# Optimization experiments

Measured on AMD Instinct MI355X. Metric: run time of the kernel, lower is better.

Reference implementation:

```python
import jax, jax.numpy as jnp
import numpy as np

THRESHOLD = 0.1   # init_kwargs threshold
CACHELINE = 64    # init_kwargs cacheline_size


def _cluster_line(line):
    """Serial near-duplicate clustering within one cacheline.

    Semantics of cluster_img's inner loops: walk the line left to right;
    each value is snapped to the FIRST earlier 'base' within THRESHOLD,
    otherwise it becomes a new base itself.
    """
    C = line.shape[0]
    slot = jnp.arange(C, dtype=jnp.int32)

    def step(carry, val):
        bases, n = carry  # bases: [C] values, n: number of valid bases
        mask = (jnp.abs(bases - val) < THRESHOLD) & (slot < n)
        has = mask.any()
        idx = jnp.argmax(mask)             # first matching base
        out = jnp.where(has, bases[idx], val)
        appended = jnp.where(slot == n, val, bases)
        bases = jnp.where(has, bases, appended)
        n = n + jnp.where(has, jnp.int32(0), jnp.int32(1))
        return (bases, n), out

    (_, _), outs = jax.lax.scan(
        step, (jnp.zeros(C, line.dtype), jnp.int32(0)), line)
    return outs


def _cluster(x):
    shape = x.shape
    flat = x.reshape(-1)
    n_lines = flat.shape[0] // CACHELINE
    head = flat[: n_lines * CACHELINE].reshape(n_lines, CACHELINE)
    clustered = jax.vmap(_cluster_line)(head).reshape(-1)
    # elements past the last full cacheline are left unchanged (while-loop tail)
    out = jnp.concatenate([clustered, flat[n_lines * CACHELINE:]])
    return out.reshape(shape)


def setup_inputs() -> dict:
    key = jax.random.key(0)
    x = jax.random.normal(key, (64, 64, 112, 112), dtype=jnp.float32)
    return {"x": x}


def reference(x):
    return _cluster(x)
```

## Files before the change

kernel.cpp:

```cpp
#include <hip/hip_runtime.h>

#define THRESH 0.1f
#define LINE 64

__global__ __launch_bounds__(256, 8) void cluster_kernel(
    const float* __restrict__ in, float* __restrict__ out,
    long long n_lines, long long total)
{
    const int lane = threadIdx.x & 63;
    const long long n_waves = ((long long)gridDim.x * blockDim.x) >> 6;
    long long line = ((long long)blockIdx.x * blockDim.x + threadIdx.x) >> 6;

    if (line < n_lines) {
        float x = in[line * LINE + lane];
        for (;;) {
            const long long next = line + n_waves;
            float xn = 0.0f;
            if (next < n_lines) xn = in[next * LINE + lane];

            float o = x;
            bool covered = false;
            unsigned long long uncovered = ~0ULL;
            while (uncovered) {
                int b = __ffsll(uncovered) - 1;
                b = __builtin_amdgcn_readfirstlane(b);
                const float base =
                    __int_as_float(__builtin_amdgcn_readlane(__float_as_int(x), b));
                const bool m = (!covered) && (fabsf(x - base) < THRESH);
                if (m) { o = base; covered = true; }
                uncovered &= ~__ballot(m);
            }
            out[line * LINE + lane] = o;

            if (next >= n_lines) break;
            x = xn;
            line = next;
        }
    }

    const long long tail_start = n_lines * LINE;
    for (long long i = tail_start + (long long)blockIdx.x * blockDim.x + threadIdx.x;
         i < total; i += (long long)gridDim.x * blockDim.x) {
        out[i] = in[i];
    }
}

extern "C" void kernel_launch(void* const* d_in, const int* in_sizes, int n_in,
                              void* d_out, int out_size, void* d_ws, size_t ws_size,
                              hipStream_t stream) {
    const float* x = (const float*)d_in[0];
    float* out = (float*)d_out;
    const long long total = (long long)in_sizes[0];
    const long long n_lines = total / LINE;

    const int block = 256;
    const int grid = 2048;
    cluster_kernel<<<grid, block, 0, stream>>>(x, out, n_lines, total);
}
```

Baseline: 553.6 us.

## Interleave two cachelines per wave in hand-written asm clustering loop

Each wavefront now processes two cachelines at once. Their serial base-selection loops run interleaved in inline GCN assembly (readlane, compare, cndmask, ff1) to expose instruction-level parallelism across the two independent dependency chains. The hand-scheduled asm also removes compiler-generated overhead from the per-iteration loop. The trade-off is that each pair runs for the longer of the two lines' iteration counts, and explicit s_nop hazard padding is added.

Result: faster. 471.0 us (-14.9%).

```diff
diff --git a/kernel.cpp b/kernel.cpp
--- a/kernel.cpp
+++ b/kernel.cpp
@@ -1,59 +1,101 @@
 #include <hip/hip_runtime.h>
 
-#define THRESH 0.1f
 #define LINE 64
+
+__device__ __forceinline__ void cluster_pair(float xA, float xB, float thr,
+                                             float& oA_out, float& oB_out) {
+  float oA = xA, oB = xB;
+  float dA, dB, vbA, vbB;
+  float sbA, sbB;
+  unsigned long long unA, unB;
+  int bA, bB;
+  asm volatile(
+      "s_mov_b64 %[unA], -1\n\t"
+      "s_mov_b64 %[unB], -1\n\t"
+      "s_mov_b32 %[bA], 0\n\t"
+      "s_mov_b32 %[bB], 0\n\t"
+      "1:\n\t"
+      "v_readlane_b32 %[sbA], %[xA], %[bA]\n\t"
+      "v_readlane_b32 %[sbB], %[xB], %[bB]\n\t"
+      "s_nop 1\n\t"
+      "v_mov_b32 %[vbA], %[sbA]\n\t"
+      "v_mov_b32 %[vbB], %[sbB]\n\t"
+      "v_sub_f32 %[dA], %[vbA], %[xA]\n\t"
+      "v_cmp_gt_f32 vcc, %[t], abs(%[dA])\n\t"
+      "s_and_b64 vcc, vcc, %[unA]\n\t"
+      "v_cndmask_b32 %[oA], %[oA], %[vbA], vcc\n\t"
+      "s_andn2_b64 %[unA], %[unA], vcc\n\t"
+      "s_ff1_i32_b64 %[bA], %[unA]\n\t"
+      "v_sub_f32 %[dB], %[vbB], %[xB]\n\t"
+      "v_cmp_gt_f32 vcc, %[t], abs(%[dB])\n\t"
+      "s_and_b64 vcc, vcc, %[unB]\n\t"
+      "v_cndmask_b32 %[oB], %[oB], %[vbB], vcc\n\t"
+      "s_andn2_b64 %[unB], %[unB], vcc\n\t"
+      "s_ff1_i32_b64 %[bB], %[unB]\n\t"
+      "s_or_b64 vcc, %[unA], %[unB]\n\t"
+      "s_cbranch_scc1 1b\n\t"
+      : [oA] "+v"(oA), [oB] "+v"(oB),
+        [dA] "=&v"(dA), [dB] "=&v"(dB),
+        [vbA] "=&v"(vbA), [vbB] "=&v"(vbB),
+        [sbA] "=&s"(sbA), [sbB] "=&s"(sbB),
+        [unA] "=&s"(unA), [unB] "=&s"(unB),
+        [bA] "=&s"(bA), [bB] "=&s"(bB)
+      : [xA] "v"(xA), [xB] "v"(xB), [t] "s"(thr)
+      : "vcc", "scc");
+  oA_out = oA;
+  oB_out = oB;
+}
 
 __global__ __launch_bounds__(256, 8) void cluster_kernel(
     const float* __restrict__ in, float* __restrict__ out,
     long long n_lines, long long total)
 {
-    const int lane = threadIdx.x & 63;
-    const long long n_waves = ((long long)gridDim.x * blockDim.x) >> 6;
-    long long line = ((long long)blockIdx.x * blockDim.x + threadIdx.x) >> 6;
+  const int lane = threadIdx.x & 63;
+  const long long wid = ((long long)blockIdx.x * blockDim.x + threadIdx.x) >> 6;
+  const long long n_waves = ((long long)gridDim.x * blockDim.x) >> 6;
+  const long long n_pairs = (n_lines + 1) >> 1;
 
-    if (line < n_lines) {
-        float x = in[line * LINE + lane];
-        for (;;) {
-            const long long next = line + n_waves;
-            float xn = 0.0f;
-            if (next < n_lines) xn = in[next * LINE + lane];
+  long long pair = wid;
+  if (pair < n_pairs) {
+    long long lA = 2 * pair, lB = 2 * pair + 1;
+    float xA = in[lA * LINE + lane];
+    float xB = (lB < n_lines) ? in[lB * LINE + lane] : xA;
+    for (;;) {
+      const long long np = pair + n_waves;
+      const bool has_next = np < n_pairs;
+      float xA2 = 0.f, xB2 = 0.f;
+      if (has_next) {
+        const long long nA = 2 * np, nB = 2 * np + 1;
+        xA2 = in[nA * LINE + lane];
+        xB2 = (nB < n_lines) ? in[nB * LINE + lane] : xA2;
+      }
 
-            float o = x;
-            bool covered = false;
-            unsigned long long uncovered = ~0ULL;
-            while (uncovered) {
-                int b = __ffsll(uncovered) - 1;
-                b = __builtin_amdgcn_readfirstlane(b);
-                const float base =
-                    __int_as_float(__builtin_amdgcn_readlane(__float_as_int(x), b));
-                const bool m = (!covered) && (fabsf(x - base) < THRESH);
-                if (m) { o = base; covered = true; }
-                uncovered &= ~__ballot(m);
-            }
-            out[line * LINE + lane] = o;
+      float oA, oB;
+      cluster_pair(xA, xB, 0.1f, oA, oB);
 
-            if (next >= n_lines) break;
-            x = xn;
-            line = next;
-        }
+      out[2 * pair * LINE + lane] = oA;
+      if (2 * pair + 1 < n_lines) out[(2 * pair + 1) * LINE + lane] = oB;
+
+      if (!has_next) break;
+      xA = xA2; xB = xB2; pair = np;
     }
+  }
 
-    const long long tail_start = n_lines * LINE;
-    for (long long i = tail_start + (long long)blockIdx.x * blockDim.x + threadIdx.x;
-         i < total; i += (long long)gridDim.x * blockDim.x) {
-        out[i] = in[i];
-    }
+  const long long tail = n_lines * LINE;
+  for (long long i = tail + (long long)blockIdx.x * blockDim.x + threadIdx.x;
+       i < total; i += (long long)gridDim.x * blockDim.x)
+    out[i] = in[i];
 }
 
 extern "C" void kernel_launch(void* const* d_in, const int* in_sizes, int n_in,
                               void* d_out, int out_size, void* d_ws, size_t ws_size,
                               hipStream_t stream) {
-    const float* x = (const float*)d_in[0];
-    float* out = (float*)d_out;
-    const long long total = (long long)in_sizes[0];
-    const long long n_lines = total / LINE;
+  const float* x = (const float*)d_in[0];
+  float* out = (float*)d_out;
+  const long long total = (long long)in_sizes[0];
+  const long long n_lines = total / LINE;
 
-    const int block = 256;
-    const int grid = 2048;
-    cluster_kernel<<<grid, block, 0, stream>>>(x, out, n_lines, total);
+  const int block = 256;
+  const int grid = 2048;
+  cluster_kernel<<<grid, block, 0, stream>>>(x, out, n_lines, total);
 }
```

## Interleave four cachelines per wave with hand-written clustering loop in asm

Applied to the files above, without the earlier changes.

Each wave now processes four consecutive cachelines at once, with the four serial base-search chains interleaved in one inline-assembly loop. Interleaving is meant to hide the latency of the readlane, compare, ballot and find-first-set chain that bounds the single-line loop. The asm also folds the bookkeeping into a few scalar mask operations. In exchange, the loop runs for the longest of the four lines' base counts, and hand-written asm risks scalar/vector hazards the compiler would normally guard against.

New measurement: 471.3 us. 1.17x faster.

```diff
diff --git a/kernel.cpp b/kernel.cpp
--- a/kernel.cpp
+++ b/kernel.cpp
@@ -1,59 +1,132 @@
 #include <hip/hip_runtime.h>
 
-#define THRESH 0.1f
 #define LINE 64
+
+__device__ __forceinline__ void cluster_quad(
+    float x0, float x1, float x2, float x3, float thr,
+    float& o0r, float& o1r, float& o2r, float& o3r) {
+  float o0 = x0, o1 = x1, o2 = x2, o3 = x3;
+  float d0, d1, d2, d3, vb0, vb1, vb2, vb3;
+  float sb0, sb1, sb2, sb3;
+  unsigned long long un0, un1, un2, un3;
+  int b0, b1, b2, b3;
+  asm volatile(
+      "s_mov_b64 %[un0], -1\n\t"
+      "s_mov_b64 %[un1], -1\n\t"
+      "s_mov_b64 %[un2], -1\n\t"
+      "s_mov_b64 %[un3], -1\n\t"
+      "s_mov_b32 %[b0], 0\n\t"
+      "s_mov_b32 %[b1], 0\n\t"
+      "s_mov_b32 %[b2], 0\n\t"
+      "s_mov_b32 %[b3], 0\n\t"
+      "1:\n\t"
+      "v_readlane_b32 %[sb0], %[x0], %[b0]\n\t"
+      "v_readlane_b32 %[sb1], %[x1], %[b1]\n\t"
+      "v_readlane_b32 %[sb2], %[x2], %[b2]\n\t"
+      "v_readlane_b32 %[sb3], %[x3], %[b3]\n\t"
+      "v_mov_b32 %[vb0], %[sb0]\n\t"
+      "v_sub_f32 %[d0], %[vb0], %[x0]\n\t"
+      "v_cmp_gt_f32 vcc, %[t], abs(%[d0])\n\t"
+      "s_and_b64 vcc, vcc, %[un0]\n\t"
+      "v_cndmask_b32 %[o0], %[o0], %[vb0], vcc\n\t"
+      "s_andn2_b64 %[un0], %[un0], vcc\n\t"
+      "s_ff1_i32_b64 %[b0], %[un0]\n\t"
+      "v_mov_b32 %[vb1], %[sb1]\n\t"
+      "v_sub_f32 %[d1], %[vb1], %[x1]\n\t"
+      "v_cmp_gt_f32 vcc, %[t], abs(%[d1])\n\t"
+      "s_and_b64 vcc, vcc, %[un1]\n\t"
+      "v_cndmask_b32 %[o1], %[o1], %[vb1], vcc\n\t"
+      "s_andn2_b64 %[un1], %[un1], vcc\n\t"
+      "s_ff1_i32_b64 %[b1], %[un1]\n\t"
+      "v_mov_b32 %[vb2], %[sb2]\n\t"
+      "v_sub_f32 %[d2], %[vb2], %[x2]\n\t"
+      "v_cmp_gt_f32 vcc, %[t], abs(%[d2])\n\t"
+      "s_and_b64 vcc, vcc, %[un2]\n\t"
+      "v_cndmask_b32 %[o2], %[o2], %[vb2], vcc\n\t"
+      "s_andn2_b64 %[un2], %[un2], vcc\n\t"
+      "s_ff1_i32_b64 %[b2], %[un2]\n\t"
+      "v_mov_b32 %[vb3], %[sb3]\n\t"
+      "v_sub_f32 %[d3], %[vb3], %[x3]\n\t"
+      "v_cmp_gt_f32 vcc, %[t], abs(%[d3])\n\t"
+      "s_and_b64 vcc, vcc, %[un3]\n\t"
+      "v_cndmask_b32 %[o3], %[o3], %[vb3], vcc\n\t"
+      "s_andn2_b64 %[un3], %[un3], vcc\n\t"
+      "s_ff1_i32_b64 %[b3], %[un3]\n\t"
+      "s_or_b64 vcc, %[un0], %[un1]\n\t"
+      "s_or_b64 vcc, vcc, %[un2]\n\t"
+      "s_or_b64 vcc, vcc, %[un3]\n\t"
+      "s_cbranch_scc1 1b\n\t"
+      : [o0] "+v"(o0), [o1] "+v"(o1), [o2] "+v"(o2), [o3] "+v"(o3),
+        [d0] "=&v"(d0), [d1] "=&v"(d1), [d2] "=&v"(d2), [d3] "=&v"(d3),
+        [vb0] "=&v"(vb0), [vb1] "=&v"(vb1), [vb2] "=&v"(vb2), [vb3] "=&v"(vb3),
+        [sb0] "=&s"(sb0), [sb1] "=&s"(sb1), [sb2] "=&s"(sb2), [sb3] "=&s"(sb3),
+        [un0] "=&s"(un0), [un1] "=&s"(un1), [un2] "=&s"(un2), [un3] "=&s"(un3),
+        [b0] "=&s"(b0), [b1] "=&s"(b1), [b2] "=&s"(b2), [b3] "=&s"(b3)
+      : [x0] "v"(x0), [x1] "v"(x1), [x2] "v"(x2), [x3] "v"(x3), [t] "s"(thr)
+      : "vcc", "scc");
+  o0r = o0; o1r = o1; o2r = o2; o3r = o3;
+}
 
 __global__ __launch_bounds__(256, 8) void cluster_kernel(
     const float* __restrict__ in, float* __restrict__ out,
     long long n_lines, long long total)
 {
-    const int lane = threadIdx.x & 63;
-    const long long n_waves = ((long long)gridDim.x * blockDim.x) >> 6;
-    long long line = ((long long)blockIdx.x * blockDim.x + threadIdx.x) >> 6;
+  const int lane = threadIdx.x & 63;
+  const long long wid = ((long long)blockIdx.x * blockDim.x + threadIdx.x) >> 6;
+  const long long n_waves = ((long long)gridDim.x * blockDim.x) >> 6;
+  const long long n_quads = (n_lines + 3) >> 2;
 
-    if (line < n_lines) {
-        float x = in[line * LINE + lane];
-        for (;;) {
-            const long long next = line + n_waves;
-            float xn = 0.0f;
-            if (next < n_lines) xn = in[next * LINE + lane];
+  long long quad = wid;
+  if (quad < n_quads) {
+    const float* p = in + quad * (4 * LINE) + lane;
+    const long long l0 = 4 * quad;
+    float x0 = p[0 * LINE];
+    float x1 = (l0 + 1 < n_lines) ? p[1 * LINE] : x0;
+    float x2 = (l0 + 2 < n_lines) ? p[2 * LINE] : x0;
+    float x3 = (l0 + 3 < n_lines) ? p[3 * LINE] : x0;
+    for (;;) {
+      const long long nq = quad + n_waves;
+      const bool has_next = nq < n_quads;
+      float y0 = 0.f, y1 = 0.f, y2 = 0.f, y3 = 0.f;
+      if (has_next) {
+        const float* pn = in + nq * (4 * LINE) + lane;
+        const long long m0 = 4 * nq;
+        y0 = pn[0 * LINE];
+        y1 = (m0 + 1 < n_lines) ? pn[1 * LINE] : y0;
+        y2 = (m0 + 2 < n_lines) ? pn[2 * LINE] : y0;
+        y3 = (m0 + 3 < n_lines) ? pn[3 * LINE] : y0;
+      }
 
-            float o = x;
-            bool covered = false;
-            unsigned long long uncovered = ~0ULL;
-            while (uncovered) {
-                int b = __ffsll(uncovered) - 1;
-                b = __builtin_amdgcn_readfirstlane(b);
-                const float base =
-                    __int_as_float(__builtin_amdgcn_readlane(__float_as_int(x), b));
-                const bool m = (!covered) && (fabsf(x - base) < THRESH);
-                if (m) { o = base; covered = true; }
-                uncovered &= ~__ballot(m);
-            }
-            out[line * LINE + lane] = o;
+      float o0, o1, o2, o3;
+      cluster_quad(x0, x1, x2, x3, 0.1f, o0, o1, o2, o3);
 
-            if (next >= n_lines) break;
-            x = xn;
-            line = next;
-        }
+      float* q = out + quad * (4 * LINE) + lane;
+      const long long c0 = 4 * quad;
+      q[0 * LINE] = o0;
+      if (c0 + 1 < n_lines) q[1 * LINE] = o1;
+      if (c0 + 2 < n_lines) q[2 * LINE] = o2;
+      if (c0 + 3 < n_lines) q[3 * LINE] = o3;
+
+      if (!has_next) break;
+      x0 = y0; x1 = y1; x2 = y2; x3 = y3; quad = nq;
     }
+  }
 
-    const long long tail_start = n_lines * LINE;
-    for (long long i = tail_start + (long long)blockIdx.x * blockDim.x + threadIdx.x;
-         i < total; i += (long long)gridDim.x * blockDim.x) {
-        out[i] = in[i];
-    }
+  const long long tail = n_lines * LINE;
+  for (long long i = tail + (long long)blockIdx.x * blockDim.x + threadIdx.x;
+       i < total; i += (long long)gridDim.x * blockDim.x)
+    out[i] = in[i];
 }
 
 extern "C" void kernel_launch(void* const* d_in, const int* in_sizes, int n_in,
                               void* d_out, int out_size, void* d_ws, size_t ws_size,
                               hipStream_t stream) {
-    const float* x = (const float*)d_in[0];
-    float* out = (float*)d_out;
-    const long long total = (long long)in_sizes[0];
-    const long long n_lines = total / LINE;
+  const float* x = (const float*)d_in[0];
+  float* out = (float*)d_out;
+  const long long total = (long long)in_sizes[0];
+  const long long n_lines = total / LINE;
 
-    const int block = 256;
-    const int grid = 2048;
-    cluster_kernel<<<grid, block, 0, stream>>>(x, out, n_lines, total);
+  const int block = 256;
+  const int grid = 2048;
+  cluster_kernel<<<grid, block, 0, stream>>>(x, out, n_lines, total);
 }
```
